# Kernel optimization log

Hardware: AMD Instinct MI355X
Metric: run time of the kernel (lower is better)

## Reference

```python
import jax, jax.numpy as jnp
import numpy as np

# ogbn-products-like 3-layer GraphSAGE mini-batch: fanouts [15, 10, 5], batch 1024
N0, N1, N2, N3 = 1_000_000, 67_584, 6_144, 1_024
F_IN, HID, OUT = 100, 256, 47
FAN1, FAN2, FAN3 = 15, 10, 5
E1, E2, E3 = N1 * FAN1, N2 * FAN2, N3 * FAN3


def _glorot(key, shape):
    lim = np.sqrt(6.0 / (shape[0] + shape[1])).astype(np.float32)
    return jax.random.uniform(key, shape, jnp.float32, -lim, lim)


def setup_inputs() -> dict:
    key = jax.random.key(0)
    ks = jax.random.split(key, 12)
    x = jax.random.normal(ks[0], (N0, F_IN), jnp.float32)
    # bipartite edge lists: src indexes into the layer's source nodes,
    # dst indexes into the first n_dst nodes (the targets)
    src1 = jax.random.randint(ks[1], (E1,), 0, N0, jnp.int64)
    dst1 = jnp.repeat(jnp.arange(N1, dtype=jnp.int64), FAN1)
    src2 = jax.random.randint(ks[2], (E2,), 0, N1, jnp.int64)
    dst2 = jnp.repeat(jnp.arange(N2, dtype=jnp.int64), FAN2)
    src3 = jax.random.randint(ks[3], (E3,), 0, N2, jnp.int64)
    dst3 = jnp.repeat(jnp.arange(N3, dtype=jnp.int64), FAN3)
    return {
        "x": x,
        "W_l1": _glorot(ks[4], (F_IN, HID)), "W_r1": _glorot(ks[5], (F_IN, HID)), "b1": jnp.zeros((HID,), jnp.float32),
        "W_l2": _glorot(ks[6], (HID, HID)), "W_r2": _glorot(ks[7], (HID, HID)), "b2": jnp.zeros((HID,), jnp.float32),
        "W_l3": _glorot(ks[8], (HID, OUT)), "W_r3": _glorot(ks[9], (HID, OUT)), "b3": jnp.zeros((OUT,), jnp.float32),
        "src1": src1, "dst1": dst1, "src2": src2, "dst2": dst2, "src3": src3, "dst3": dst3,
    }


def _sage_conv(x_src, x_dst, src, dst, W_l, W_r, b, n_dst):
    # mean aggregation over incoming edges, then out = lin_l(agg) + lin_r(x_dst)
    msg = x_src[src]                                             # [E, d]
    agg = jax.ops.segment_sum(msg, dst, num_segments=n_dst)      # [n_dst, d]
    cnt = jax.ops.segment_sum(jnp.ones((src.shape[0],), x_src.dtype), dst,
                              num_segments=n_dst)
    agg = agg / jnp.maximum(cnt, 1.0)[:, None]
    return agg @ W_l + x_dst @ W_r + b


def reference(x, W_l1, W_r1, b1, W_l2, W_r2, b2, W_l3, W_r3, b3,
              src1, dst1, src2, dst2, src3, dst3):
    h = _sage_conv(x, x[:N1], src1, dst1, W_l1, W_r1, b1, N1)
    h = jax.nn.relu(h)                                           # dropout in eval mode = identity
    h = _sage_conv(h, h[:N2], src2, dst2, W_l2, W_r2, b2, N2)
    h = jax.nn.relu(h)
    h = _sage_conv(h, h[:N3], src3, dst3, W_l3, W_r3, b3, N3)
    return jax.nn.log_softmax(h, axis=-1)                        # [N3, OUT]
```

## Files before the change

### kernel.cpp

```cpp
#include <hip/hip_runtime.h>
#include <math.h>

static constexpr int cN1 = 67584, cN2 = 6144, cN3 = 1024;
static constexpr int F_IN = 100, HID = 256, OUT = 47;
static constexpr int K1P = 224;

typedef __attribute__((ext_vector_type(8))) short short8;
typedef __attribute__((ext_vector_type(4))) float float4v;

__device__ __forceinline__ ushort f2b(float f) {
    unsigned u = __builtin_bit_cast(unsigned, f);
    u += 0x7fff + ((u >> 16) & 1);
    return (ushort)(u >> 16);
}
__device__ __forceinline__ unsigned pack2(float a, float b) {
    return (unsigned)f2b(a) | ((unsigned)f2b(b) << 16);
}

__global__ void build_A1(const float* __restrict__ x, const int* __restrict__ src,
                         ushort* __restrict__ A1)
{
    int wave = (int)((blockIdx.x * blockDim.x + threadIdx.x) >> 6);
    int lane = threadIdx.x & 63;
    if (wave >= cN1) return;
    const int* s = src + (size_t)wave * 15;
    const int half = lane >> 5, hl = lane & 31;
    const bool act = hl < 25;
    float4 own = {0.f, 0.f, 0.f, 0.f};
    if (half == 1 && act)
        own = *(const float4*)(x + (size_t)wave * F_IN + 4 * hl);
    float4 acc = {0.f, 0.f, 0.f, 0.f};
    #pragma unroll
    for (int j = 0; j < 8; ++j) {
        int e = 2 * j + half;
        if (e < 15 && act) {
            float4 v = *(const float4*)(x + (size_t)s[e] * F_IN + 4 * hl);
            acc.x += v.x; acc.y += v.y; acc.z += v.z; acc.w += v.w;
        }
    }
    acc.x += __shfl(acc.x, lane ^ 32);
    acc.y += __shfl(acc.y, lane ^ 32);
    acc.z += __shfl(acc.z, lane ^ 32);
    acc.w += __shfl(acc.w, lane ^ 32);
    ushort* outp = A1 + (size_t)wave * K1P;
    constexpr float inv = 1.0f / 15.0f;
    if (half == 0) {
        if (act) {
            ushort4 m; m.x = f2b(acc.x * inv); m.y = f2b(acc.y * inv);
                       m.z = f2b(acc.z * inv); m.w = f2b(acc.w * inv);
            *(ushort4*)(outp + 4 * hl) = m;
        }
    } else {
        if (act) {
            ushort4 d; d.x = f2b(own.x); d.y = f2b(own.y); d.z = f2b(own.z); d.w = f2b(own.w);
            *(ushort4*)(outp + 100 + 4 * hl) = d;
        } else if (hl < 31) {
            ushort4 z; z.x = 0; z.y = 0; z.z = 0; z.w = 0;
            *(ushort4*)(outp + 200 + 4 * (hl - 25)) = z;
        }
    }
}

template<int FAN>
__global__ void build_A(const ushort* __restrict__ H, const int* __restrict__ src,
                        ushort* __restrict__ A, int M)
{
    int wave = (int)((blockIdx.x * blockDim.x + threadIdx.x) >> 6);
    int lane = threadIdx.x & 63;
    if (wave >= M) return;
    const int* s = src + (size_t)wave * FAN;
    const int half = lane >> 5, hl = lane & 31;
    const float* Hf = (const float*)H;
    float4 own;
    if (half == 1)
        own = *(const float4*)(Hf + (size_t)wave * 128 + 4 * hl);
    float a[8] = {0.f, 0.f, 0.f, 0.f, 0.f, 0.f, 0.f, 0.f};
    constexpr int NJ = (FAN + 1) / 2;
    #pragma unroll
    for (int j = 0; j < NJ; ++j) {
        int e = 2 * j + half;
        if (e < FAN) {
            float4 v = *(const float4*)(Hf + (size_t)s[e] * 128 + 4 * hl);
            unsigned u;
            u = __builtin_bit_cast(unsigned, v.x);
            a[0] += __builtin_bit_cast(float, u << 16); a[1] += __builtin_bit_cast(float, u & 0xffff0000u);
            u = __builtin_bit_cast(unsigned, v.y);
            a[2] += __builtin_bit_cast(float, u << 16); a[3] += __builtin_bit_cast(float, u & 0xffff0000u);
            u = __builtin_bit_cast(unsigned, v.z);
            a[4] += __builtin_bit_cast(float, u << 16); a[5] += __builtin_bit_cast(float, u & 0xffff0000u);
            u = __builtin_bit_cast(unsigned, v.w);
            a[6] += __builtin_bit_cast(float, u << 16); a[7] += __builtin_bit_cast(float, u & 0xffff0000u);
        }
    }
    #pragma unroll
    for (int i = 0; i < 8; ++i) a[i] += __shfl(a[i], lane ^ 32);
    ushort* outp = A + (size_t)wave * (2 * HID);
    constexpr float inv = 1.0f / (float)FAN;
    if (half == 0) {
        uint4 w;
        w.x = pack2(a[0] * inv, a[1] * inv);
        w.y = pack2(a[2] * inv, a[3] * inv);
        w.z = pack2(a[4] * inv, a[5] * inv);
        w.w = pack2(a[6] * inv, a[7] * inv);
        *(uint4*)(outp + 8 * hl) = w;
    } else {
        *(float4*)(outp + HID + 8 * hl) = own;
    }
}

static constexpr int S1 = 256 * K1P, S2 = 256 * 512, S3 = 128 * 512;
__global__ void conv_W_all(const float* __restrict__ Wl1, const float* __restrict__ Wr1,
                           const float* __restrict__ Wl2, const float* __restrict__ Wr2,
                           const float* __restrict__ Wl3, const float* __restrict__ Wr3,
                           ushort* __restrict__ Bt1, ushort* __restrict__ Bt2,
                           ushort* __restrict__ Bt3)
{
    int idx = blockIdx.x * 256 + threadIdx.x;
    if (idx < S1) {
        int n = idx / K1P, k = idx - n * K1P;
        float v = 0.f;
        if (k < 100)      v = Wl1[(size_t)k * 256 + n];
        else if (k < 200) v = Wr1[(size_t)(k - 100) * 256 + n];
        Bt1[idx] = f2b(v);
    } else if (idx < S1 + S2) {
        int i = idx - S1;
        int n = i >> 9, k = i & 511;
        float v = (k < 256) ? Wl2[(size_t)k * 256 + n] : Wr2[(size_t)(k - 256) * 256 + n];
        Bt2[i] = f2b(v);
    } else if (idx < S1 + S2 + S3) {
        int i = idx - S1 - S2;
        int n = i >> 9, k = i & 511;
        float v = 0.f;
        if (n < OUT) v = (k < 256) ? Wl3[(size_t)k * OUT + n] : Wr3[(size_t)(k - 256) * OUT + n];
        Bt3[i] = f2b(v);
    }
}

template<bool OUT_BF16, bool RELU, bool LS>
__launch_bounds__(256)
__global__ void mfma_gemm(const ushort* __restrict__ A, const ushort* __restrict__ Bt,
                          const float* __restrict__ bias, void* __restrict__ Cout,
                          int M, int N, int K)
{
    constexpr int BM = 128, BK = 32, SA = BK + 8;
    __shared__ ushort As[BM * SA];
    __shared__ ushort Bs[BM * SA];
    const int tid  = threadIdx.x;
    const int m0   = blockIdx.y * BM;
    const int n0   = blockIdx.x * BM;
    const int lane = tid & 63;
    const int w    = tid >> 6;
    const int wr   = (w >> 1) * 64;
    const int wc   = (w & 1) * 64;
    const int m_in = lane & 15;
    const int k8   = (lane >> 4) * 8;
    const int srow = tid >> 1;
    const int skc  = (tid & 1) * 16;

    float4v acc[4][4] = {};

    const ushort* gA = A  + (size_t)(m0 + srow) * K + skc;
    const ushort* gB = Bt + (size_t)(n0 + srow) * K + skc;

    for (int k0 = 0; k0 < K; k0 += BK) {
        float4 a0 = ((const float4*)(gA + k0))[0];
        float4 a1 = ((const float4*)(gA + k0))[1];
        float4 b0 = ((const float4*)(gB + k0))[0];
        float4 b1 = ((const float4*)(gB + k0))[1];
        __syncthreads();
        *(float4*)&As[srow * SA + skc]     = a0;
        *(float4*)&As[srow * SA + skc + 8] = a1;
        *(float4*)&Bs[srow * SA + skc]     = b0;
        *(float4*)&Bs[srow * SA + skc + 8] = b1;
        __syncthreads();
        short8 af[4], bf[4];
        #pragma unroll
        for (int i = 0; i < 4; ++i) {
            af[i] = *(const short8*)&As[(wr + i * 16 + m_in) * SA + k8];
            bf[i] = *(const short8*)&Bs[(wc + i * 16 + m_in) * SA + k8];
        }
        #pragma unroll
        for (int mi = 0; mi < 4; ++mi)
            #pragma unroll
            for (int ni = 0; ni < 4; ++ni)
                acc[mi][ni] = __builtin_amdgcn_mfma_f32_16x16x32_bf16(af[mi], bf[ni], acc[mi][ni], 0, 0, 0);
    }

    if (LS) {
        if (wc != 0) return;
        #pragma unroll
        for (int mi = 0; mi < 4; ++mi) {
            #pragma unroll
            for (int r = 0; r < 4; ++r) {
                float v[4]; float mx = -3.0e38f;
                #pragma unroll
                for (int ni = 0; ni < 4; ++ni) {
                    int col = ni * 16 + m_in;
                    v[ni] = (col < N) ? acc[mi][ni][r] + bias[col] : -3.0e38f;
                    mx = fmaxf(mx, v[ni]);
                }
                #pragma unroll
                for (int off = 1; off < 16; off <<= 1) mx = fmaxf(mx, __shfl_xor(mx, off));
                float sum = 0.f;
                #pragma unroll
                for (int ni = 0; ni < 4; ++ni)
                    sum += (v[ni] > -1.0e38f) ? expf(v[ni] - mx) : 0.f;
                #pragma unroll
                for (int off = 1; off < 16; off <<= 1) sum += __shfl_xor(sum, off);
                float ls = logf(sum);
                int row = m0 + wr + mi * 16 + (lane >> 4) * 4 + r;
                #pragma unroll
                for (int ni = 0; ni < 4; ++ni) {
                    int col = ni * 16 + m_in;
                    if (col < N)
                        ((float*)Cout)[(size_t)row * N + col] = v[ni] - mx - ls;
                }
            }
        }
        return;
    }

    #pragma unroll
    for (int ni = 0; ni < 4; ++ni) {
        int col = n0 + wc + ni * 16 + m_in;
        if (col >= N) continue;
        float bv = bias[col];
        #pragma unroll
        for (int mi = 0; mi < 4; ++mi) {
            #pragma unroll
            for (int r = 0; r < 4; ++r) {
                int row = m0 + wr + mi * 16 + (lane >> 4) * 4 + r;
                float v = acc[mi][ni][r] + bv;
                if (RELU) v = fmaxf(v, 0.f);
                if (OUT_BF16) ((ushort*)Cout)[(size_t)row * N + col] = f2b(v);
                else          ((float*)Cout)[(size_t)row * N + col] = v;
            }
        }
    }
}

extern "C" void kernel_launch(void* const* d_in, const int* in_sizes, int n_in,
                              void* d_out, int out_size, void* d_ws, size_t ws_size,
                              hipStream_t stream)
{
    const float* x    = (const float*)d_in[0];
    const float* W_l1 = (const float*)d_in[1];
    const float* W_r1 = (const float*)d_in[2];
    const float* b1   = (const float*)d_in[3];
    const float* W_l2 = (const float*)d_in[4];
    const float* W_r2 = (const float*)d_in[5];
    const float* b2   = (const float*)d_in[6];
    const float* W_l3 = (const float*)d_in[7];
    const float* W_r3 = (const float*)d_in[8];
    const float* b3   = (const float*)d_in[9];
    const int* src1 = (const int*)d_in[10];
    const int* src2 = (const int*)d_in[12];
    const int* src3 = (const int*)d_in[14];
    float* out = (float*)d_out;

    ushort* ws  = (ushort*)d_ws;
    ushort* A1  = ws;
    ushort* h1  = A1  + (size_t)cN1 * K1P;
    ushort* A2  = h1  + (size_t)cN1 * HID;
    ushort* h2  = A2  + (size_t)cN2 * 2 * HID;
    ushort* A3  = h2  + (size_t)cN2 * HID;
    ushort* Bt1 = A3  + (size_t)cN3 * 2 * HID;
    ushort* Bt2 = Bt1 + (size_t)256 * K1P;
    ushort* Bt3 = Bt2 + (size_t)256 * 2 * HID;

    conv_W_all<<<(S1 + S2 + S3 + 255) / 256, 256, 0, stream>>>(
        W_l1, W_r1, W_l2, W_r2, W_l3, W_r3, Bt1, Bt2, Bt3);

    build_A1<<<cN1 / 4, 256, 0, stream>>>(x, src1, A1);
    mfma_gemm<true, true, false><<<dim3(2, cN1 / 128), 256, 0, stream>>>(A1, Bt1, b1, h1, cN1, HID, K1P);
    build_A<10><<<cN2 / 4, 256, 0, stream>>>(h1, src2, A2, cN2);
    mfma_gemm<true, true, false><<<dim3(2, cN2 / 128), 256, 0, stream>>>(A2, Bt2, b2, h2, cN2, HID, 512);
    build_A<5><<<cN3 / 4, 256, 0, stream>>>(h2, src3, A3, cN3);
    mfma_gemm<false, false, true><<<dim3(1, cN3 / 128), 256, 0, stream>>>(A3, Bt3, b3, out, cN3, OUT, 512);
}
```

Measured before the change: 654.6 us.

## Fuse layer-1 gather/mean with MFMA GEMM through shared memory

Replaces the separate build_A1 kernel and the layer-1 GEMM with one fused kernel. Each 512-thread block gathers and averages neighbor features for 128 rows into LDS as bf16, runs MFMA against the transposed weights, then applies bias and ReLU and writes h1 through LDS with coalesced stores. This removes the A1 round trip through global memory and one launch. In exchange it uses 64KB of LDS per block, which lowers occupancy, and each block runs its gather and GEMM phases one after the other with no overlap between them.

Result: slower. 865.8 us (+32.3%).

```diff
diff --git a/kernel.cpp b/kernel.cpp
--- a/kernel.cpp
+++ b/kernel.cpp
@@ -17,47 +17,95 @@
     return (unsigned)f2b(a) | ((unsigned)f2b(b) << 16);
 }
 
-__global__ void build_A1(const float* __restrict__ x, const int* __restrict__ src,
-                         ushort* __restrict__ A1)
-{
-    int wave = (int)((blockIdx.x * blockDim.x + threadIdx.x) >> 6);
-    int lane = threadIdx.x & 63;
-    if (wave >= cN1) return;
-    const int* s = src + (size_t)wave * 15;
+__launch_bounds__(512)
+__global__ void fused_l1(const float* __restrict__ x, const int* __restrict__ src,
+                         const ushort* __restrict__ Bt, const float* __restrict__ bias,
+                         ushort* __restrict__ h1)
+{
+    __shared__ ushort lds[128 * 256];
+    constexpr int SA = 232;
+    const int tid  = threadIdx.x;
+    const int lane = tid & 63, w = tid >> 6;
+    const int m0   = blockIdx.x * 128;
     const int half = lane >> 5, hl = lane & 31;
     const bool act = hl < 25;
-    float4 own = {0.f, 0.f, 0.f, 0.f};
-    if (half == 1 && act)
-        own = *(const float4*)(x + (size_t)wave * F_IN + 4 * hl);
-    float4 acc = {0.f, 0.f, 0.f, 0.f};
-    #pragma unroll
-    for (int j = 0; j < 8; ++j) {
-        int e = 2 * j + half;
-        if (e < 15 && act) {
-            float4 v = *(const float4*)(x + (size_t)s[e] * F_IN + 4 * hl);
-            acc.x += v.x; acc.y += v.y; acc.z += v.z; acc.w += v.w;
-        }
-    }
-    acc.x += __shfl(acc.x, lane ^ 32);
-    acc.y += __shfl(acc.y, lane ^ 32);
-    acc.z += __shfl(acc.z, lane ^ 32);
-    acc.w += __shfl(acc.w, lane ^ 32);
-    ushort* outp = A1 + (size_t)wave * K1P;
-    constexpr float inv = 1.0f / 15.0f;
-    if (half == 0) {
-        if (act) {
-            ushort4 m; m.x = f2b(acc.x * inv); m.y = f2b(acc.y * inv);
-                       m.z = f2b(acc.z * inv); m.w = f2b(acc.w * inv);
-            *(ushort4*)(outp + 4 * hl) = m;
-        }
-    } else {
-        if (act) {
-            ushort4 d; d.x = f2b(own.x); d.y = f2b(own.y); d.z = f2b(own.z); d.w = f2b(own.w);
-            *(ushort4*)(outp + 100 + 4 * hl) = d;
-        } else if (hl < 31) {
-            ushort4 z; z.x = 0; z.y = 0; z.z = 0; z.w = 0;
-            *(ushort4*)(outp + 200 + 4 * (hl - 25)) = z;
-        }
+
+    for (int i = 0; i < 16; ++i) {
+        const int rl  = 16 * w + i;
+        const int row = m0 + rl;
+        const int* s  = src + (size_t)row * 15;
+        float4 acc = {0.f, 0.f, 0.f, 0.f};
+        float4 own = {0.f, 0.f, 0.f, 0.f};
+        if (half == 1 && act)
+            own = *(const float4*)(x + (size_t)row * F_IN + 4 * hl);
+        #pragma unroll
+        for (int j = 0; j < 8; ++j) {
+            int e = 2 * j + half;
+            if (e < 15 && act) {
+                float4 v = *(const float4*)(x + (size_t)s[e] * F_IN + 4 * hl);
+                acc.x += v.x; acc.y += v.y; acc.z += v.z; acc.w += v.w;
+            }
+        }
+        acc.x += __shfl(acc.x, lane ^ 32);
+        acc.y += __shfl(acc.y, lane ^ 32);
+        acc.z += __shfl(acc.z, lane ^ 32);
+        acc.w += __shfl(acc.w, lane ^ 32);
+        ushort* outp = &lds[rl * SA];
+        constexpr float inv = 1.0f / 15.0f;
+        if (half == 0) {
+            if (act) {
+                ushort4 m; m.x = f2b(acc.x * inv); m.y = f2b(acc.y * inv);
+                           m.z = f2b(acc.z * inv); m.w = f2b(acc.w * inv);
+                *(ushort4*)(outp + 4 * hl) = m;
+            }
+        } else {
+            if (act) {
+                ushort4 d; d.x = f2b(own.x); d.y = f2b(own.y); d.z = f2b(own.z); d.w = f2b(own.w);
+                *(ushort4*)(outp + 100 + 4 * hl) = d;
+            } else if (hl < 31) {
+                ushort4 z; z.x = 0; z.y = 0; z.z = 0; z.w = 0;
+                *(ushort4*)(outp + 200 + 4 * (hl - 25)) = z;
+            }
+        }
+    }
+    __syncthreads();
+
+    const int wr = (w >> 2) * 64, wc = (w & 3) * 64;
+    const int m_in = lane & 15, k8 = (lane >> 4) * 8;
+    float4v acc[4][4] = {};
+    for (int k0 = 0; k0 < K1P; k0 += 32) {
+        short8 af[4], bf[4];
+        #pragma unroll
+        for (int i = 0; i < 4; ++i) {
+            af[i] = *(const short8*)&lds[(wr + i * 16 + m_in) * SA + k0 + k8];
+            bf[i] = *(const short8*)(Bt + (size_t)(wc + i * 16 + m_in) * K1P + k0 + k8);
+        }
+        #pragma unroll
+        for (int mi = 0; mi < 4; ++mi)
+            #pragma unroll
+            for (int ni = 0; ni < 4; ++ni)
+                acc[mi][ni] = __builtin_amdgcn_mfma_f32_16x16x32_bf16(af[mi], bf[ni], acc[mi][ni], 0, 0, 0);
+    }
+    __syncthreads();
+
+    #pragma unroll
+    for (int ni = 0; ni < 4; ++ni) {
+        int col = wc + ni * 16 + m_in;
+        float bv = bias[col];
+        #pragma unroll
+        for (int mi = 0; mi < 4; ++mi)
+            #pragma unroll
+            for (int r = 0; r < 4; ++r) {
+                int row = wr + mi * 16 + (lane >> 4) * 4 + r;
+                lds[row * 256 + col] = f2b(fmaxf(acc[mi][ni][r] + bv, 0.f));
+            }
+    }
+    __syncthreads();
+    #pragma unroll
+    for (int p = 0; p < 8; ++p) {
+        int rl = p * 16 + (tid >> 5);
+        int c  = (tid & 31) * 8;
+        *(uint4*)(h1 + (size_t)(m0 + rl) * 256 + c) = *(const uint4*)&lds[rl * 256 + c];
     }
 }
 
@@ -71,7 +119,7 @@
     const int* s = src + (size_t)wave * FAN;
     const int half = lane >> 5, hl = lane & 31;
     const float* Hf = (const float*)H;
-    float4 own;
+    float4 own = {0.f, 0.f, 0.f, 0.f};
     if (half == 1)
         own = *(const float4*)(Hf + (size_t)wave * 128 + 4 * hl);
     float a[8] = {0.f, 0.f, 0.f, 0.f, 0.f, 0.f, 0.f, 0.f};
@@ -97,12 +145,12 @@
     ushort* outp = A + (size_t)wave * (2 * HID);
     constexpr float inv = 1.0f / (float)FAN;
     if (half == 0) {
-        uint4 w;
-        w.x = pack2(a[0] * inv, a[1] * inv);
-        w.y = pack2(a[2] * inv, a[3] * inv);
-        w.z = pack2(a[4] * inv, a[5] * inv);
-        w.w = pack2(a[6] * inv, a[7] * inv);
-        *(uint4*)(outp + 8 * hl) = w;
+        uint4 wv;
+        wv.x = pack2(a[0] * inv, a[1] * inv);
+        wv.y = pack2(a[2] * inv, a[3] * inv);
+        wv.z = pack2(a[4] * inv, a[5] * inv);
+        wv.w = pack2(a[6] * inv, a[7] * inv);
+        *(uint4*)(outp + 8 * hl) = wv;
     } else {
         *(float4*)(outp + HID + 8 * hl) = own;
     }
@@ -226,7 +274,7 @@
         if (col >= N) continue;
         float bv = bias[col];
         #pragma unroll
-        for (int mi = 0; mi < 4; ++mi) {
+        for (int mi = 0; mi < 4; ++mi)
             #pragma unroll
             for (int r = 0; r < 4; ++r) {
                 int row = m0 + wr + mi * 16 + (lane >> 4) * 4 + r;
@@ -235,7 +283,6 @@
                 if (OUT_BF16) ((ushort*)Cout)[(size_t)row * N + col] = f2b(v);
                 else          ((float*)Cout)[(size_t)row * N + col] = v;
             }
-        }
     }
 }
 
@@ -259,8 +306,7 @@
     float* out = (float*)d_out;
 
     ushort* ws  = (ushort*)d_ws;
-    ushort* A1  = ws;
-    ushort* h1  = A1  + (size_t)cN1 * K1P;
+    ushort* h1  = ws;
     ushort* A2  = h1  + (size_t)cN1 * HID;
     ushort* h2  = A2  + (size_t)cN2 * 2 * HID;
     ushort* A3  = h2  + (size_t)cN2 * HID;
@@ -271,8 +317,7 @@
     conv_W_all<<<(S1 + S2 + S3 + 255) / 256, 256, 0, stream>>>(
         W_l1, W_r1, W_l2, W_r2, W_l3, W_r3, Bt1, Bt2, Bt3);
 
-    build_A1<<<cN1 / 4, 256, 0, stream>>>(x, src1, A1);
-    mfma_gemm<true, true, false><<<dim3(2, cN1 / 128), 256, 0, stream>>>(A1, Bt1, b1, h1, cN1, HID, K1P);
+    fused_l1<<<cN1 / 128, 512, 0, stream>>>(x, src1, Bt1, b1, h1);
     build_A<10><<<cN2 / 4, 256, 0, stream>>>(h1, src2, A2, cN2);
     mfma_gemm<true, true, false><<<dim3(2, cN2 / 128), 256, 0, stream>>>(A2, Bt2, b2, h2, cN2, HID, 512);
     build_A<5><<<cN3 / 4, 256, 0, stream>>>(h2, src3, A3, cN3);
```
